# Performance work log

Measured on AMD Instinct MI355X. Metric: run time of the kernel, lower is better.

Reference implementation:

```python
import jax, jax.numpy as jnp
import numpy as np

BN_EPS = 1e-5


def setup_inputs() -> dict:
    key = jax.random.key(0)
    ks = jax.random.split(key, 8)
    N, E, D, G, L = 50000, 800000, 128, 64, 4
    x = jax.random.normal(ks[0], (N, D), dtype=jnp.float32)
    edge_index = jax.random.randint(ks[1], (2, E), 0, N, dtype=jnp.int64)
    batch = jnp.sort(jax.random.randint(ks[2], (N,), 0, G, dtype=jnp.int64))
    sc = 1.0 / np.sqrt(D)
    W1 = jax.random.normal(ks[3], (L, D, D), dtype=jnp.float32) * sc
    b1 = jnp.zeros((L, D), dtype=jnp.float32)
    gamma = jnp.ones((L, D), dtype=jnp.float32)
    beta = jnp.zeros((L, D), dtype=jnp.float32)
    W2 = jax.random.normal(ks[4], (L, D, D), dtype=jnp.float32) * sc
    b2 = jnp.zeros((L, D), dtype=jnp.float32)
    return {"x": x, "edge_index": edge_index, "batch": batch,
            "W1": W1, "b1": b1, "gamma": gamma, "beta": beta,
            "W2": W2, "b2": b2}


def _segment_mean(vals, ids, num_segments):
    s = jax.ops.segment_sum(vals, ids, num_segments=num_segments)
    cnt = jax.ops.segment_sum(jnp.ones((vals.shape[0],), vals.dtype), ids,
                              num_segments=num_segments)
    return s / jnp.clip(cnt, 1.0)[:, None]


def reference(x, edge_index, batch, W1, b1, gamma, beta, W2, b2):
    N = x.shape[0]
    L = W1.shape[0]
    G = 64  # number of graphs
    src, dst = edge_index[0], edge_index[1]  # source_to_target flow
    # in-degree counts for scatter-mean (fixed across layers)
    deg = jax.ops.segment_sum(jnp.ones((src.shape[0],), x.dtype), dst,
                              num_segments=N)
    deg = jnp.clip(deg, 1.0)[:, None]
    h = x
    node_pool = jnp.zeros((N, W1.shape[2]), x.dtype)
    g_pool = jnp.zeros((G, W1.shape[2]), x.dtype)
    for l in range(L):
        # scatter-mean neighbor aggregation, GIN update with eps=0
        agg = jax.ops.segment_sum(h[src], dst, num_segments=N) / deg
        z = h + agg
        # MLP: Linear -> BatchNorm1d (batch stats) -> ReLU -> Linear
        z = z @ W1[l] + b1[l]
        mu = jnp.mean(z, axis=0)
        var = jnp.mean(jnp.square(z - mu), axis=0)  # biased, as in torch BN
        z = gamma[l] * (z - mu) * jax.lax.rsqrt(var + BN_EPS) + beta[l]
        z = jax.nn.relu(z)
        h = z @ W2[l] + b2[l]
        node_pool = node_pool + h
        g_pool = g_pool + _segment_mean(h, batch, G)
    return node_pool, g_pool
```

## Files before the change

### kernel.cpp

```cpp
#include <hip/hip_runtime.h>

#define D 128
#define GNUM 64
#define LNUM 4
#define BN_EPS 1e-5f
#define EPB 16384
#define SH_MAX 12544

typedef short bf16x8 __attribute__((ext_vector_type(8)));
typedef float f32x4 __attribute__((ext_vector_type(4)));
typedef unsigned short u16x8 __attribute__((ext_vector_type(8)));
typedef unsigned short u16x4 __attribute__((ext_vector_type(4)));

__device__ __forceinline__ float bf2f(unsigned short u) {
  union { unsigned int i; float f; } v; v.i = ((unsigned int)u) << 16; return v.f;
}
__device__ __forceinline__ unsigned short f2bf(float f) {
  union { float f; unsigned int i; } v; v.f = f;
  unsigned int b = v.i;
  return (unsigned short)((b + 0x7FFFu + ((b >> 16) & 1u)) >> 16);
}


__global__ __launch_bounds__(256) void k_hist(const int* __restrict__ ei, int E,
                                              int B, int nbin, int* __restrict__ hist) {
  __shared__ int lh[256];
  int b = blockIdx.x, tx = threadIdx.x;
  lh[tx] = 0;
  __syncthreads();
  int s = b * EPB, e = min(s + EPB, E);
  for (int j = s + tx; j < e; j += 256) atomicAdd(&lh[ei[(size_t)E + j] >> 8], 1);
  __syncthreads();
  if (tx < nbin) hist[tx * B + b] = lh[tx];
}

__global__ __launch_bounds__(1024) void k_hscan(const int* __restrict__ hist, int M,
                                                int* __restrict__ off,
                                                int* __restrict__ rowptr, int N, int E) {
  __shared__ int sh[SH_MAX];
  __shared__ int sh2[1024];
  int tx = threadIdx.x;
  int chunk = (M + 1023) / 1024;
  for (int i = 0; i < chunk; ++i) {
    int idx = tx * chunk + i;
    sh[idx] = (idx < M) ? hist[idx] : 0;
  }
  __syncthreads();
  int s = 0;
  for (int i = 0; i < chunk; ++i) s += sh[tx * chunk + i];
  sh2[tx] = s;
  __syncthreads();
  for (int o = 1; o < 1024; o <<= 1) {
    int u = (tx >= o) ? sh2[tx - o] : 0;
    __syncthreads();
    sh2[tx] += u;
    __syncthreads();
  }
  int run = (tx == 0) ? 0 : sh2[tx - 1];
  for (int i = 0; i < chunk; ++i) {
    int idx = tx * chunk + i;
    if (idx < M) { int v = sh[idx]; off[idx] = run; run += v; }
  }
  if (tx == 0) rowptr[N] = E;
}

__global__ __launch_bounds__(256) void k_scatter(const int* __restrict__ ei, int E,
                                                 int B, int nbin,
                                                 const int* __restrict__ off,
                                                 int2* __restrict__ sorted) {
  __shared__ int cur[256];
  int b = blockIdx.x, tx = threadIdx.x;
  if (tx < nbin) cur[tx] = off[tx * B + b];
  __syncthreads();
  int s = b * EPB, e = min(s + EPB, E);
  for (int j = s + tx; j < e; j += 256) {
    int d = ei[(size_t)E + j];
    int sc = ei[j];
    int p = atomicAdd(&cur[d >> 8], 1);
    sorted[p] = make_int2(d, sc);
  }
}

__global__ __launch_bounds__(256) void k_build(const int2* __restrict__ sorted,
                                               const int* __restrict__ off,
                                               int B, int nbin, int E, int N,
                                               int* __restrict__ rowptr,
                                               int* __restrict__ col) {
  __shared__ int cnt[256], excl[256], cur[256];
  int beta = blockIdx.x, tx = threadIdx.x;
  int s = off[beta * B];
  int e = (beta + 1 < nbin) ? off[(beta + 1) * B] : E;
  cnt[tx] = 0;
  __syncthreads();
  for (int j = s + tx; j < e; j += 256) atomicAdd(&cnt[sorted[j].x & 255], 1);
  __syncthreads();
  int v = cnt[tx];
  excl[tx] = v;
  __syncthreads();
  for (int o = 1; o < 256; o <<= 1) {
    int u = (tx >= o) ? excl[tx - o] : 0;
    __syncthreads();
    excl[tx] += u;
    __syncthreads();
  }
  int ex = excl[tx] - v;
  int n = beta * 256 + tx;
  if (n < N) rowptr[n] = s + ex;
  cur[tx] = s + ex;
  __syncthreads();
  for (int j = s + tx; j < e; j += 256) {
    int2 p = sorted[j];
    int q = atomicAdd(&cur[p.x & 255], 1);
    col[q] = p.y;
  }
}

__global__ void k_bounds(const int* __restrict__ batch, int N, int* __restrict__ bound) {
  int g = threadIdx.x;
  if (g > GNUM) return;
  int lo = 0, hi = N;
  while (lo < hi) { int mid = (lo + hi) >> 1; if (batch[mid] < g) lo = mid + 1; else hi = mid; }
  bound[g] = lo;
}

__global__ void k_prep_x(const float* __restrict__ x, unsigned short* __restrict__ hx, int total4) {
  int i = blockIdx.x * 256 + threadIdx.x;
  if (i < total4) {
    f32x4 v = ((const f32x4*)x)[i];
    u16x4 o; o[0] = f2bf(v[0]); o[1] = f2bf(v[1]); o[2] = f2bf(v[2]); o[3] = f2bf(v[3]);
    ((u16x4*)hx)[i] = o;
  }
}

__global__ __launch_bounds__(256) void k_prep_w(const float* __restrict__ W1,
                                                const float* __restrict__ W2,
                                                unsigned short* __restrict__ wt) {
  int l = blockIdx.x;
  const float* W = (l < LNUM) ? (W1 + (size_t)l * D * D) : (W2 + (size_t)(l - LNUM) * D * D);
  unsigned short* o = wt + (size_t)l * D * D;
#pragma unroll
  for (int i = 0; i < 64; ++i) {
    int idx = threadIdx.x + 256 * i;
    int k = idx >> 7, n = idx & 127;
    o[n * D + k] = f2bf(W[idx]);
  }
}

__global__ __launch_bounds__(256) void k_aggz(const unsigned short* __restrict__ hin,
                                              const int* __restrict__ rowptr,
                                              const int* __restrict__ col,
                                              int N, unsigned short* __restrict__ z) {
  int tx = threadIdx.x;
  int w = tx >> 6, l = tx & 63;
  int g = l >> 4;
  int c = l & 15;
  int n = blockIdx.x * 4 + w;
  if (n >= N) return;
  int e0 = rowptr[n], e1 = rowptr[n + 1];
  const u16x8* h8 = (const u16x8*)hin;
  f32x4 a0 = {0.f, 0.f, 0.f, 0.f}, a1 = {0.f, 0.f, 0.f, 0.f};
  f32x4 b0 = {0.f, 0.f, 0.f, 0.f}, b1 = {0.f, 0.f, 0.f, 0.f};
  int j = e0 + g;
  for (; j + 4 < e1; j += 8) {
    int cj0 = col[j];
    int cj1 = col[j + 4];
    u16x8 v0 = h8[(size_t)cj0 * 16 + c];
    u16x8 v1 = h8[(size_t)cj1 * 16 + c];
    a0[0] += bf2f(v0[0]); a0[1] += bf2f(v0[1]); a0[2] += bf2f(v0[2]); a0[3] += bf2f(v0[3]);
    a1[0] += bf2f(v0[4]); a1[1] += bf2f(v0[5]); a1[2] += bf2f(v0[6]); a1[3] += bf2f(v0[7]);
    b0[0] += bf2f(v1[0]); b0[1] += bf2f(v1[1]); b0[2] += bf2f(v1[2]); b0[3] += bf2f(v1[3]);
    b1[0] += bf2f(v1[4]); b1[1] += bf2f(v1[5]); b1[2] += bf2f(v1[6]); b1[3] += bf2f(v1[7]);
  }
  if (j < e1) {
    int cj = col[j];
    u16x8 v = h8[(size_t)cj * 16 + c];
    a0[0] += bf2f(v[0]); a0[1] += bf2f(v[1]); a0[2] += bf2f(v[2]); a0[3] += bf2f(v[3]);
    a1[0] += bf2f(v[4]); a1[1] += bf2f(v[5]); a1[2] += bf2f(v[6]); a1[3] += bf2f(v[7]);
  }
  a0 += b0; a1 += b1;
#pragma unroll
  for (int m = 16; m <= 32; m <<= 1) {
#pragma unroll
    for (int i = 0; i < 4; ++i) {
      a0[i] += __shfl_xor(a0[i], m, 64);
      a1[i] += __shfl_xor(a1[i], m, 64);
    }
  }
  if (g == 0) {
    float inv = (e1 > e0) ? 1.f / (float)(e1 - e0) : 0.f;
    u16x8 hv = h8[(size_t)n * 16 + c];
    u16x8 o;
    o[0] = f2bf(bf2f(hv[0]) + a0[0] * inv);
    o[1] = f2bf(bf2f(hv[1]) + a0[1] * inv);
    o[2] = f2bf(bf2f(hv[2]) + a0[2] * inv);
    o[3] = f2bf(bf2f(hv[3]) + a0[3] * inv);
    o[4] = f2bf(bf2f(hv[4]) + a1[0] * inv);
    o[5] = f2bf(bf2f(hv[5]) + a1[1] * inv);
    o[6] = f2bf(bf2f(hv[6]) + a1[2] * inv);
    o[7] = f2bf(bf2f(hv[7]) + a1[3] * inv);
    ((u16x8*)z)[(size_t)n * 16 + c] = o;
  }
}

__global__ __launch_bounds__(256) void k_gemm1(const unsigned short* __restrict__ z,
                                               const unsigned short* __restrict__ wt,
                                               const float* __restrict__ bias,
                                               unsigned short* __restrict__ t,
                                               float* __restrict__ partials, int N) {
  __shared__ union { unsigned short zt[64 * D]; float red[2 * 8 * D]; } uA;
  __shared__ union { unsigned short wl[D * D]; float out[64 * D]; } uB;
  int tx = threadIdx.x;
  int r0 = blockIdx.x * 64;
  const u16x8* zg = (const u16x8*)(z + (size_t)r0 * D);
#pragma unroll
  for (int i = 0; i < 4; ++i) {
    int cid = tx + 256 * i;
    int row = cid >> 4, c16 = cid & 15;
    u16x8 v = zg[cid];
    *(u16x8*)((char*)uA.zt + row * 256 + ((c16 * 16) ^ ((row & 7) << 4))) = v;
  }
  const u16x8* wg = (const u16x8*)wt;
#pragma unroll
  for (int i = 0; i < 8; ++i) {
    int cid = tx + 256 * i;
    int row = cid >> 4, c16 = cid & 15;
    u16x8 v = wg[cid];
    *(u16x8*)((char*)uB.wl + row * 256 + ((c16 * 16) ^ ((row & 7) << 4))) = v;
  }
  __syncthreads();
  int l = tx & 63, w = tx >> 6;
  int lm = l & 15, lg = l >> 4;
  f32x4 acc[8];
#pragma unroll
  for (int c = 0; c < 8; ++c) { float bv = bias[c * 16 + lm]; acc[c] = (f32x4){bv, bv, bv, bv}; }
  int arow = 16 * w + lm;
  const char* zb = (const char*)uA.zt + arow * 256;
  int aswz = (arow & 7) << 4;
#pragma unroll
  for (int kt = 0; kt < 4; ++kt) {
    int koff = kt * 64 + lg * 16;
    bf16x8 af = *(const bf16x8*)(zb + (koff ^ aswz));
#pragma unroll
    for (int c = 0; c < 8; ++c) {
      int n = c * 16 + lm;
      bf16x8 bfr = *(const bf16x8*)((const char*)uB.wl + n * 256 + (koff ^ ((n & 7) << 4)));
      acc[c] = __builtin_amdgcn_mfma_f32_16x16x32_bf16(af, bfr, acc[c], 0, 0, 0);
    }
  }
  __syncthreads();
#pragma unroll
  for (int c = 0; c < 8; ++c)
#pragma unroll
    for (int r = 0; r < 4; ++r)
      uB.out[(16 * w + 4 * lg + r) * D + c * 16 + lm] = acc[c][r];
  __syncthreads();
  int tc = tx & 31, tr = tx >> 5;
  f32x4 s = {0.f, 0.f, 0.f, 0.f}, q = {0.f, 0.f, 0.f, 0.f};
#pragma unroll
  for (int i = 0; i < 8; ++i) {
    int row = i * 8 + tr;
    f32x4 v = *(f32x4*)&uB.out[row * D + tc * 4];
    u16x4 o; o[0] = f2bf(v[0]); o[1] = f2bf(v[1]); o[2] = f2bf(v[2]); o[3] = f2bf(v[3]);
    *(u16x4*)(t + (size_t)(r0 + row) * D + tc * 4) = o;
    if (r0 + row < N) { s += v; q += v * v; }
  }
  *(f32x4*)&uA.red[tr * D + tc * 4] = s;
  *(f32x4*)&uA.red[8 * D + tr * D + tc * 4] = q;
  __syncthreads();
  int colx = tx & 127, which = tx >> 7;
  float S = 0.f;
#pragma unroll
  for (int j = 0; j < 8; ++j) S += uA.red[which * 8 * D + j * D + colx];
  partials[(size_t)blockIdx.x * 256 + tx] = S;
}

__global__ __launch_bounds__(256) void k_red1(const float* __restrict__ partials, int NB,
                                              float* __restrict__ partial2) {
  int tx = threadIdx.x;
  float S = 0.f;
  for (int b = blockIdx.x; b < NB; b += 64) S += partials[(size_t)b * 256 + tx];
  partial2[(size_t)blockIdx.x * 256 + tx] = S;
}

__global__ __launch_bounds__(256) void k_finalize(const float* __restrict__ partial2,
                                                  const float* __restrict__ gamma,
                                                  const float* __restrict__ beta,
                                                  float* __restrict__ stats, int N) {
  __shared__ float sh[256];
  int tx = threadIdx.x;
  float S = 0.f;
#pragma unroll 8
  for (int b = 0; b < 64; ++b) S += partial2[(size_t)b * 256 + tx];
  sh[tx] = S;
  __syncthreads();
  if (tx < D) {
    float mu = sh[tx] / (float)N;
    float var = sh[D + tx] / (float)N - mu * mu;
    float rstd = rsqrtf(fmaxf(var, 0.f) + BN_EPS);
    float A = gamma[tx] * rstd;
    stats[tx] = A;
    stats[D + tx] = beta[tx] - mu * A;
  }
}

__global__ __launch_bounds__(256) void k_gemm2(const unsigned short* __restrict__ t,
                                               const unsigned short* __restrict__ wt,
                                               const float* __restrict__ bias,
                                               const float* __restrict__ stats,
                                               unsigned short* __restrict__ h,
                                               float* __restrict__ node_pool, int N) {
  __shared__ unsigned short at[64 * D];
  __shared__ union { unsigned short wl[D * D]; float out[64 * D]; } uB;
  int tx = threadIdx.x;
  int r0 = blockIdx.x * 64;
  const u16x8* tg = (const u16x8*)(t + (size_t)r0 * D);
#pragma unroll
  for (int i = 0; i < 4; ++i) {
    int cid = tx + 256 * i;
    int row = cid >> 4, c16 = cid & 15;
    u16x8 v = tg[cid];
    int c0 = c16 * 8;
    f32x4 a0 = *(const f32x4*)&stats[c0];
    f32x4 a1 = *(const f32x4*)&stats[c0 + 4];
    f32x4 b0 = *(const f32x4*)&stats[D + c0];
    f32x4 b1v = *(const f32x4*)&stats[D + c0 + 4];
    u16x8 o;
    o[0] = f2bf(fmaxf(bf2f(v[0]) * a0[0] + b0[0], 0.f));
    o[1] = f2bf(fmaxf(bf2f(v[1]) * a0[1] + b0[1], 0.f));
    o[2] = f2bf(fmaxf(bf2f(v[2]) * a0[2] + b0[2], 0.f));
    o[3] = f2bf(fmaxf(bf2f(v[3]) * a0[3] + b0[3], 0.f));
    o[4] = f2bf(fmaxf(bf2f(v[4]) * a1[0] + b1v[0], 0.f));
    o[5] = f2bf(fmaxf(bf2f(v[5]) * a1[1] + b1v[1], 0.f));
    o[6] = f2bf(fmaxf(bf2f(v[6]) * a1[2] + b1v[2], 0.f));
    o[7] = f2bf(fmaxf(bf2f(v[7]) * a1[3] + b1v[3], 0.f));
    *(u16x8*)((char*)at + row * 256 + ((c16 * 16) ^ ((row & 7) << 4))) = o;
  }
  const u16x8* wg = (const u16x8*)wt;
#pragma unroll
  for (int i = 0; i < 8; ++i) {
    int cid = tx + 256 * i;
    int row = cid >> 4, c16 = cid & 15;
    u16x8 v = wg[cid];
    *(u16x8*)((char*)uB.wl + row * 256 + ((c16 * 16) ^ ((row & 7) << 4))) = v;
  }
  __syncthreads();
  int l = tx & 63, w = tx >> 6;
  int lm = l & 15, lg = l >> 4;
  f32x4 acc[8];
#pragma unroll
  for (int c = 0; c < 8; ++c) { float bv = bias[c * 16 + lm]; acc[c] = (f32x4){bv, bv, bv, bv}; }
  int arow = 16 * w + lm;
  const char* ab = (const char*)at + arow * 256;
  int aswz = (arow & 7) << 4;
#pragma unroll
  for (int kt = 0; kt < 4; ++kt) {
    int koff = kt * 64 + lg * 16;
    bf16x8 af = *(const bf16x8*)(ab + (koff ^ aswz));
#pragma unroll
    for (int c = 0; c < 8; ++c) {
      int n = c * 16 + lm;
      bf16x8 bfr = *(const bf16x8*)((const char*)uB.wl + n * 256 + (koff ^ ((n & 7) << 4)));
      acc[c] = __builtin_amdgcn_mfma_f32_16x16x32_bf16(af, bfr, acc[c], 0, 0, 0);
    }
  }
  __syncthreads();
#pragma unroll
  for (int c = 0; c < 8; ++c)
#pragma unroll
    for (int r = 0; r < 4; ++r)
      uB.out[(16 * w + 4 * lg + r) * D + c * 16 + lm] = acc[c][r];
  __syncthreads();
  int tc = tx & 31, tr = tx >> 5;
#pragma unroll
  for (int i = 0; i < 8; ++i) {
    int row = i * 8 + tr;
    int gr = r0 + row;
    if (gr < N) {
      f32x4 v = *(f32x4*)&uB.out[row * D + tc * 4];
      f32x4* np = (f32x4*)(node_pool + (size_t)gr * D + tc * 4);
      f32x4 o = *np;
      o += v;
      *np = o;
      u16x4 hb; hb[0] = f2bf(v[0]); hb[1] = f2bf(v[1]); hb[2] = f2bf(v[2]); hb[3] = f2bf(v[3]);
      *(u16x4*)(h + (size_t)gr * D + tc * 4) = hb;
    }
  }
}

__global__ __launch_bounds__(256) void k_gpool(const float* __restrict__ np,
                                               const int* __restrict__ bound,
                                               float* __restrict__ gp) {
  __shared__ float red[8 * D];
  int g = blockIdx.x;
  int s = bound[g], e = bound[g + 1];
  int tc = threadIdx.x & 31, tr = threadIdx.x >> 5;
  f32x4 a = {0.f, 0.f, 0.f, 0.f};
  for (int r = s + tr; r < e; r += 8)
    a += *(const f32x4*)(np + (size_t)r * D + tc * 4);
  *(f32x4*)&red[tr * D + tc * 4] = a;
  __syncthreads();
  if (threadIdx.x < D) {
    float v = 0.f;
#pragma unroll
    for (int j = 0; j < 8; ++j) v += red[j * D + threadIdx.x];
    float c = (float)(e - s);
    gp[(size_t)g * D + threadIdx.x] = v / fmaxf(c, 1.f);
  }
}

extern "C" void kernel_launch(void* const* d_in, const int* in_sizes, int n_in,
                              void* d_out, int out_size, void* d_ws,
                              size_t ws_size, hipStream_t stream) {
  const float* x = (const float*)d_in[0];
  const int* ei = (const int*)d_in[1];
  const int* batch = (const int*)d_in[2];
  const float* W1 = (const float*)d_in[3];
  const float* b1 = (const float*)d_in[4];
  const float* gamma = (const float*)d_in[5];
  const float* beta = (const float*)d_in[6];
  const float* W2 = (const float*)d_in[7];
  const float* b2 = (const float*)d_in[8];
  int N = in_sizes[0] / D;
  int E = in_sizes[1] / 2;
  int Npad = (N + 63) & ~63;
  int gb = Npad / 64;
  int B = (E + EPB - 1) / EPB;
  int nbin = (N + 255) / 256;
  int M = nbin * B;

  float* out = (float*)d_out;
  float* node_pool = out;
  float* g_pool = out + (size_t)N * D;

  char* wp = (char*)d_ws;
  unsigned short* t_hx = (unsigned short*)wp; wp += (size_t)Npad * D * 2;
  unsigned short* h = (unsigned short*)wp;    wp += (size_t)Npad * D * 2;
  unsigned short* z = (unsigned short*)wp;    wp += (size_t)Npad * D * 2;
  unsigned short* wt = (unsigned short*)wp;   wp += (size_t)8 * D * D * 2;
  float* partials = (float*)wp;               wp += (size_t)gb * 256 * 4;
  float* partial2 = (float*)wp;               wp += (size_t)64 * 256 * 4;
  float* stats = (float*)wp;                  wp += (size_t)2 * D * 4;
  int* bound = (int*)wp;                      wp += (size_t)(GNUM + 4) * 4;
  int* rowptr = (int*)wp;                     wp += (size_t)(N + 1) * 4;
  int* hist = (int*)wp;                       wp += (size_t)SH_MAX * 4;
  int* off = (int*)wp;                        wp += (size_t)SH_MAX * 4;
  int* col = (int*)wp;                        wp += (size_t)E * 4;
  int2* sorted = (int2*)wp;                   wp += (size_t)E * 8;

  hipMemsetAsync(node_pool, 0, (size_t)N * D * 4, stream);
  if (Npad > N) {
    size_t padB = (size_t)(Npad - N) * D * 2;
    hipMemsetAsync(t_hx + (size_t)N * D, 0, padB, stream);
    hipMemsetAsync(h + (size_t)N * D, 0, padB, stream);
    hipMemsetAsync(z + (size_t)N * D, 0, padB, stream);
  }

  k_prep_w<<<8, 256, 0, stream>>>(W1, W2, wt);
  k_prep_x<<<(N * 32 + 255) / 256, 256, 0, stream>>>(x, t_hx, N * 32);
  k_hist<<<B, 256, 0, stream>>>(ei, E, B, nbin, hist);
  k_hscan<<<1, 1024, 0, stream>>>(hist, M, off, rowptr, N, E);
  k_scatter<<<B, 256, 0, stream>>>(ei, E, B, nbin, off, sorted);
  k_build<<<nbin, 256, 0, stream>>>(sorted, off, B, nbin, E, N, rowptr, col);
  k_bounds<<<1, 128, 0, stream>>>(batch, N, bound);

  int ab = (N + 3) / 4;
  for (int ll = 0; ll < LNUM; ++ll) {
    const unsigned short* hin = (ll == 0) ? t_hx : h;
    k_aggz<<<ab, 256, 0, stream>>>(hin, rowptr, col, N, z);
    k_gemm1<<<gb, 256, 0, stream>>>(z, wt + (size_t)ll * D * D, b1 + (size_t)ll * D,
                                    t_hx, partials, N);
    k_red1<<<64, 256, 0, stream>>>(partials, gb, partial2);
    k_finalize<<<1, 256, 0, stream>>>(partial2, gamma + (size_t)ll * D,
                                      beta + (size_t)ll * D, stats, N);
    k_gemm2<<<gb, 256, 0, stream>>>(t_hx, wt + (size_t)(LNUM + ll) * D * D,
                                    b2 + (size_t)ll * D, stats, h, node_pool, N);
  }
  k_gpool<<<GNUM, 256, 0, stream>>>(node_pool, bound, g_pool);
}
```

Before: 450.4 us.

## Defer node_pool accumulation to one final kernel and unroll neighbor gather

Each layer's bf16 output h now goes to its own buffer, and k_gemm2 no longer does a read-modify-write of the fp32 node_pool. A new k_npool kernel sums the four bf16 layer outputs once at the end and writes node_pool, which also removes the zeroing memset of node_pool. The aggregation loop in k_aggz is unrolled to four independent neighbor loads and accumulators per iteration, giving more loads in flight. The cost is more workspace, and node_pool is now summed from bf16-rounded h rather than fp32 values, which slightly lowers precision.

```diff
diff --git a/kernel.cpp b/kernel.cpp
--- a/kernel.cpp
+++ b/kernel.cpp
@@ -160,24 +160,35 @@
   const u16x8* h8 = (const u16x8*)hin;
   f32x4 a0 = {0.f, 0.f, 0.f, 0.f}, a1 = {0.f, 0.f, 0.f, 0.f};
   f32x4 b0 = {0.f, 0.f, 0.f, 0.f}, b1 = {0.f, 0.f, 0.f, 0.f};
+  f32x4 c0 = {0.f, 0.f, 0.f, 0.f}, c1 = {0.f, 0.f, 0.f, 0.f};
+  f32x4 d0 = {0.f, 0.f, 0.f, 0.f}, d1 = {0.f, 0.f, 0.f, 0.f};
   int j = e0 + g;
-  for (; j + 4 < e1; j += 8) {
+  for (; j + 12 < e1; j += 16) {
     int cj0 = col[j];
     int cj1 = col[j + 4];
+    int cj2 = col[j + 8];
+    int cj3 = col[j + 12];
     u16x8 v0 = h8[(size_t)cj0 * 16 + c];
     u16x8 v1 = h8[(size_t)cj1 * 16 + c];
+    u16x8 v2 = h8[(size_t)cj2 * 16 + c];
+    u16x8 v3 = h8[(size_t)cj3 * 16 + c];
     a0[0] += bf2f(v0[0]); a0[1] += bf2f(v0[1]); a0[2] += bf2f(v0[2]); a0[3] += bf2f(v0[3]);
     a1[0] += bf2f(v0[4]); a1[1] += bf2f(v0[5]); a1[2] += bf2f(v0[6]); a1[3] += bf2f(v0[7]);
     b0[0] += bf2f(v1[0]); b0[1] += bf2f(v1[1]); b0[2] += bf2f(v1[2]); b0[3] += bf2f(v1[3]);
     b1[0] += bf2f(v1[4]); b1[1] += bf2f(v1[5]); b1[2] += bf2f(v1[6]); b1[3] += bf2f(v1[7]);
-  }
-  if (j < e1) {
+    c0[0] += bf2f(v2[0]); c0[1] += bf2f(v2[1]); c0[2] += bf2f(v2[2]); c0[3] += bf2f(v2[3]);
+    c1[0] += bf2f(v2[4]); c1[1] += bf2f(v2[5]); c1[2] += bf2f(v2[6]); c1[3] += bf2f(v2[7]);
+    d0[0] += bf2f(v3[0]); d0[1] += bf2f(v3[1]); d0[2] += bf2f(v3[2]); d0[3] += bf2f(v3[3]);
+    d1[0] += bf2f(v3[4]); d1[1] += bf2f(v3[5]); d1[2] += bf2f(v3[6]); d1[3] += bf2f(v3[7]);
+  }
+  for (; j < e1; j += 4) {
     int cj = col[j];
     u16x8 v = h8[(size_t)cj * 16 + c];
     a0[0] += bf2f(v[0]); a0[1] += bf2f(v[1]); a0[2] += bf2f(v[2]); a0[3] += bf2f(v[3]);
     a1[0] += bf2f(v[4]); a1[1] += bf2f(v[5]); a1[2] += bf2f(v[6]); a1[3] += bf2f(v[7]);
   }
-  a0 += b0; a1 += b1;
+  a0 += b0; c0 += d0; a0 += c0;
+  a1 += b1; c1 += d1; a1 += c1;
 #pragma unroll
   for (int m = 16; m <= 32; m <<= 1) {
 #pragma unroll
@@ -307,8 +318,7 @@
                                                const unsigned short* __restrict__ wt,
                                                const float* __restrict__ bias,
                                                const float* __restrict__ stats,
-                                               unsigned short* __restrict__ h,
-                                               float* __restrict__ node_pool, int N) {
+                                               unsigned short* __restrict__ h, int N) {
   __shared__ unsigned short at[64 * D];
   __shared__ union { unsigned short wl[D * D]; float out[64 * D]; } uB;
   int tx = threadIdx.x;
@@ -377,14 +387,31 @@
     int gr = r0 + row;
     if (gr < N) {
       f32x4 v = *(f32x4*)&uB.out[row * D + tc * 4];
-      f32x4* np = (f32x4*)(node_pool + (size_t)gr * D + tc * 4);
-      f32x4 o = *np;
-      o += v;
-      *np = o;
       u16x4 hb; hb[0] = f2bf(v[0]); hb[1] = f2bf(v[1]); hb[2] = f2bf(v[2]); hb[3] = f2bf(v[3]);
       *(u16x4*)(h + (size_t)gr * D + tc * 4) = hb;
     }
   }
+}
+
+__global__ void k_npool(const unsigned short* __restrict__ h0,
+                        const unsigned short* __restrict__ h1,
+                        const unsigned short* __restrict__ h2,
+                        const unsigned short* __restrict__ h3,
+                        float* __restrict__ np, int total8) {
+  int i = blockIdx.x * 256 + threadIdx.x;
+  if (i >= total8) return;
+  u16x8 a = ((const u16x8*)h0)[i];
+  u16x8 b = ((const u16x8*)h1)[i];
+  u16x8 c = ((const u16x8*)h2)[i];
+  u16x8 d = ((const u16x8*)h3)[i];
+  f32x4 lo, hi;
+#pragma unroll
+  for (int j = 0; j < 4; ++j) {
+    lo[j] = (bf2f(a[j]) + bf2f(b[j])) + (bf2f(c[j]) + bf2f(d[j]));
+    hi[j] = (bf2f(a[4 + j]) + bf2f(b[4 + j])) + (bf2f(c[4 + j]) + bf2f(d[4 + j]));
+  }
+  ((f32x4*)np)[2 * i] = lo;
+  ((f32x4*)np)[2 * i + 1] = hi;
 }
 
 __global__ __launch_bounds__(256) void k_gpool(const float* __restrict__ np,
@@ -434,8 +461,9 @@
 
   char* wp = (char*)d_ws;
   unsigned short* t_hx = (unsigned short*)wp; wp += (size_t)Npad * D * 2;
-  unsigned short* h = (unsigned short*)wp;    wp += (size_t)Npad * D * 2;
   unsigned short* z = (unsigned short*)wp;    wp += (size_t)Npad * D * 2;
+  unsigned short* hbuf[LNUM];
+  for (int l = 0; l < LNUM; ++l) { hbuf[l] = (unsigned short*)wp; wp += (size_t)Npad * D * 2; }
   unsigned short* wt = (unsigned short*)wp;   wp += (size_t)8 * D * D * 2;
   float* partials = (float*)wp;               wp += (size_t)gb * 256 * 4;
   float* partial2 = (float*)wp;               wp += (size_t)64 * 256 * 4;
@@ -447,12 +475,8 @@
   int* col = (int*)wp;                        wp += (size_t)E * 4;
   int2* sorted = (int2*)wp;                   wp += (size_t)E * 8;
 
-  hipMemsetAsync(node_pool, 0, (size_t)N * D * 4, stream);
   if (Npad > N) {
-    size_t padB = (size_t)(Npad - N) * D * 2;
-    hipMemsetAsync(t_hx + (size_t)N * D, 0, padB, stream);
-    hipMemsetAsync(h + (size_t)N * D, 0, padB, stream);
-    hipMemsetAsync(z + (size_t)N * D, 0, padB, stream);
+    hipMemsetAsync(z + (size_t)N * D, 0, (size_t)(Npad - N) * D * 2, stream);
   }
 
   k_prep_w<<<8, 256, 0, stream>>>(W1, W2, wt);
@@ -465,7 +489,7 @@
 
   int ab = (N + 3) / 4;
   for (int ll = 0; ll < LNUM; ++ll) {
-    const unsigned short* hin = (ll == 0) ? t_hx : h;
+    const unsigned short* hin = (ll == 0) ? t_hx : hbuf[ll - 1];
     k_aggz<<<ab, 256, 0, stream>>>(hin, rowptr, col, N, z);
     k_gemm1<<<gb, 256, 0, stream>>>(z, wt + (size_t)ll * D * D, b1 + (size_t)ll * D,
                                     t_hx, partials, N);
@@ -473,7 +497,10 @@
     k_finalize<<<1, 256, 0, stream>>>(partial2, gamma + (size_t)ll * D,
                                       beta + (size_t)ll * D, stats, N);
     k_gemm2<<<gb, 256, 0, stream>>>(t_hx, wt + (size_t)(LNUM + ll) * D * D,
-                                    b2 + (size_t)ll * D, stats, h, node_pool, N);
-  }
+                                    b2 + (size_t)ll * D, stats, hbuf[ll], N);
+  }
+  int total8 = N * (D / 8);
+  k_npool<<<(total8 + 255) / 256, 256, 0, stream>>>(hbuf[0], hbuf[1], hbuf[2], hbuf[3],
+                                                    node_pool, total8);
   k_gpool<<<GNUM, 256, 0, stream>>>(node_pool, bound, g_pool);
 }
```

After: 458.7 us. Within noise of the previous version (+1.8%).

## Fuse neighbor aggregation into first GEMM and defer node_pool accumulation

Applied to the files above, without the earlier changes.

Aggregation of neighbor features is moved into the first GEMM kernel, so each block gathers its 64 rows directly into shared memory instead of going through a global z buffer. Per-layer fp32 node_pool read-modify-write is replaced by keeping each layer's bf16 output in its own buffer and summing all four in the final GEMM2 epilogue. This removes z round-trips, several memsets, and three full fp32 RMW passes. In exchange, gather parallelism per row drops and LDS-heavy blocks may limit latency hiding, and earlier-layer contributions to node_pool are bf16-rounded.

```diff
diff --git a/kernel.cpp b/kernel.cpp
--- a/kernel.cpp
+++ b/kernel.cpp
@@ -20,7 +20,6 @@
   unsigned int b = v.i;
   return (unsigned short)((b + 0x7FFFu + ((b >> 16) & 1u)) >> 16);
 }
-
 
 __global__ __launch_bounds__(256) void k_hist(const int* __restrict__ ei, int E,
                                               int B, int nbin, int* __restrict__ hist) {
@@ -146,79 +145,17 @@
   }
 }
 
-__global__ __launch_bounds__(256) void k_aggz(const unsigned short* __restrict__ hin,
-                                              const int* __restrict__ rowptr,
-                                              const int* __restrict__ col,
-                                              int N, unsigned short* __restrict__ z) {
-  int tx = threadIdx.x;
-  int w = tx >> 6, l = tx & 63;
-  int g = l >> 4;
-  int c = l & 15;
-  int n = blockIdx.x * 4 + w;
-  if (n >= N) return;
-  int e0 = rowptr[n], e1 = rowptr[n + 1];
-  const u16x8* h8 = (const u16x8*)hin;
-  f32x4 a0 = {0.f, 0.f, 0.f, 0.f}, a1 = {0.f, 0.f, 0.f, 0.f};
-  f32x4 b0 = {0.f, 0.f, 0.f, 0.f}, b1 = {0.f, 0.f, 0.f, 0.f};
-  int j = e0 + g;
-  for (; j + 4 < e1; j += 8) {
-    int cj0 = col[j];
-    int cj1 = col[j + 4];
-    u16x8 v0 = h8[(size_t)cj0 * 16 + c];
-    u16x8 v1 = h8[(size_t)cj1 * 16 + c];
-    a0[0] += bf2f(v0[0]); a0[1] += bf2f(v0[1]); a0[2] += bf2f(v0[2]); a0[3] += bf2f(v0[3]);
-    a1[0] += bf2f(v0[4]); a1[1] += bf2f(v0[5]); a1[2] += bf2f(v0[6]); a1[3] += bf2f(v0[7]);
-    b0[0] += bf2f(v1[0]); b0[1] += bf2f(v1[1]); b0[2] += bf2f(v1[2]); b0[3] += bf2f(v1[3]);
-    b1[0] += bf2f(v1[4]); b1[1] += bf2f(v1[5]); b1[2] += bf2f(v1[6]); b1[3] += bf2f(v1[7]);
-  }
-  if (j < e1) {
-    int cj = col[j];
-    u16x8 v = h8[(size_t)cj * 16 + c];
-    a0[0] += bf2f(v[0]); a0[1] += bf2f(v[1]); a0[2] += bf2f(v[2]); a0[3] += bf2f(v[3]);
-    a1[0] += bf2f(v[4]); a1[1] += bf2f(v[5]); a1[2] += bf2f(v[6]); a1[3] += bf2f(v[7]);
-  }
-  a0 += b0; a1 += b1;
-#pragma unroll
-  for (int m = 16; m <= 32; m <<= 1) {
-#pragma unroll
-    for (int i = 0; i < 4; ++i) {
-      a0[i] += __shfl_xor(a0[i], m, 64);
-      a1[i] += __shfl_xor(a1[i], m, 64);
-    }
-  }
-  if (g == 0) {
-    float inv = (e1 > e0) ? 1.f / (float)(e1 - e0) : 0.f;
-    u16x8 hv = h8[(size_t)n * 16 + c];
-    u16x8 o;
-    o[0] = f2bf(bf2f(hv[0]) + a0[0] * inv);
-    o[1] = f2bf(bf2f(hv[1]) + a0[1] * inv);
-    o[2] = f2bf(bf2f(hv[2]) + a0[2] * inv);
-    o[3] = f2bf(bf2f(hv[3]) + a0[3] * inv);
-    o[4] = f2bf(bf2f(hv[4]) + a1[0] * inv);
-    o[5] = f2bf(bf2f(hv[5]) + a1[1] * inv);
-    o[6] = f2bf(bf2f(hv[6]) + a1[2] * inv);
-    o[7] = f2bf(bf2f(hv[7]) + a1[3] * inv);
-    ((u16x8*)z)[(size_t)n * 16 + c] = o;
-  }
-}
-
-__global__ __launch_bounds__(256) void k_gemm1(const unsigned short* __restrict__ z,
-                                               const unsigned short* __restrict__ wt,
-                                               const float* __restrict__ bias,
-                                               unsigned short* __restrict__ t,
-                                               float* __restrict__ partials, int N) {
+__global__ __launch_bounds__(256) void k_layer1(const unsigned short* __restrict__ hin,
+                                                const int* __restrict__ rowptr,
+                                                const int* __restrict__ col,
+                                                const unsigned short* __restrict__ wt,
+                                                const float* __restrict__ bias,
+                                                unsigned short* __restrict__ t,
+                                                float* __restrict__ partials, int N) {
   __shared__ union { unsigned short zt[64 * D]; float red[2 * 8 * D]; } uA;
   __shared__ union { unsigned short wl[D * D]; float out[64 * D]; } uB;
   int tx = threadIdx.x;
   int r0 = blockIdx.x * 64;
-  const u16x8* zg = (const u16x8*)(z + (size_t)r0 * D);
-#pragma unroll
-  for (int i = 0; i < 4; ++i) {
-    int cid = tx + 256 * i;
-    int row = cid >> 4, c16 = cid & 15;
-    u16x8 v = zg[cid];
-    *(u16x8*)((char*)uA.zt + row * 256 + ((c16 * 16) ^ ((row & 7) << 4))) = v;
-  }
   const u16x8* wg = (const u16x8*)wt;
 #pragma unroll
   for (int i = 0; i < 8; ++i) {
@@ -227,12 +164,55 @@
     u16x8 v = wg[cid];
     *(u16x8*)((char*)uB.wl + row * 256 + ((c16 * 16) ^ ((row & 7) << 4))) = v;
   }
+  int grp = tx >> 4, c = tx & 15;
+  const u16x8* h8 = (const u16x8*)hin;
+#pragma unroll
+  for (int i = 0; i < 4; ++i) {
+    int row = grp * 4 + i;
+    int n = r0 + row;
+    u16x8 o;
+    if (n < N) {
+      int e0 = rowptr[n], e1 = rowptr[n + 1];
+      f32x4 s0 = {0.f,0.f,0.f,0.f}, s1 = {0.f,0.f,0.f,0.f};
+      f32x4 t0 = {0.f,0.f,0.f,0.f}, t1 = {0.f,0.f,0.f,0.f};
+      int j = e0;
+      for (; j + 3 < e1; j += 4) {
+        u16x8 v0 = h8[(size_t)col[j] * 16 + c];
+        u16x8 v1 = h8[(size_t)col[j + 1] * 16 + c];
+        u16x8 v2 = h8[(size_t)col[j + 2] * 16 + c];
+        u16x8 v3 = h8[(size_t)col[j + 3] * 16 + c];
+#pragma unroll
+        for (int k = 0; k < 4; ++k) {
+          s0[k] += bf2f(v0[k]) + bf2f(v1[k]);
+          s1[k] += bf2f(v0[4 + k]) + bf2f(v1[4 + k]);
+          t0[k] += bf2f(v2[k]) + bf2f(v3[k]);
+          t1[k] += bf2f(v2[4 + k]) + bf2f(v3[4 + k]);
+        }
+      }
+      for (; j < e1; ++j) {
+        u16x8 v0 = h8[(size_t)col[j] * 16 + c];
+#pragma unroll
+        for (int k = 0; k < 4; ++k) { s0[k] += bf2f(v0[k]); s1[k] += bf2f(v0[4 + k]); }
+      }
+      s0 += t0; s1 += t1;
+      float inv = (e1 > e0) ? 1.f / (float)(e1 - e0) : 0.f;
+      u16x8 hv = h8[(size_t)n * 16 + c];
+#pragma unroll
+      for (int k = 0; k < 4; ++k) {
+        o[k] = f2bf(bf2f(hv[k]) + s0[k] * inv);
+        o[4 + k] = f2bf(bf2f(hv[4 + k]) + s1[k] * inv);
+      }
+    } else {
+      o = (u16x8){0, 0, 0, 0, 0, 0, 0, 0};
+    }
+    *(u16x8*)((char*)uA.zt + row * 256 + ((c * 16) ^ ((row & 7) << 4))) = o;
+  }
   __syncthreads();
   int l = tx & 63, w = tx >> 6;
   int lm = l & 15, lg = l >> 4;
   f32x4 acc[8];
 #pragma unroll
-  for (int c = 0; c < 8; ++c) { float bv = bias[c * 16 + lm]; acc[c] = (f32x4){bv, bv, bv, bv}; }
+  for (int cc = 0; cc < 8; ++cc) { float bv = bias[cc * 16 + lm]; acc[cc] = (f32x4){bv, bv, bv, bv}; }
   int arow = 16 * w + lm;
   const char* zb = (const char*)uA.zt + arow * 256;
   int aswz = (arow & 7) << 4;
@@ -241,18 +221,18 @@
     int koff = kt * 64 + lg * 16;
     bf16x8 af = *(const bf16x8*)(zb + (koff ^ aswz));
 #pragma unroll
-    for (int c = 0; c < 8; ++c) {
-      int n = c * 16 + lm;
+    for (int cc = 0; cc < 8; ++cc) {
+      int n = cc * 16 + lm;
       bf16x8 bfr = *(const bf16x8*)((const char*)uB.wl + n * 256 + (koff ^ ((n & 7) << 4)));
-      acc[c] = __builtin_amdgcn_mfma_f32_16x16x32_bf16(af, bfr, acc[c], 0, 0, 0);
-    }
-  }
-  __syncthreads();
-#pragma unroll
-  for (int c = 0; c < 8; ++c)
+      acc[cc] = __builtin_amdgcn_mfma_f32_16x16x32_bf16(af, bfr, acc[cc], 0, 0, 0);
+    }
+  }
+  __syncthreads();
+#pragma unroll
+  for (int cc = 0; cc < 8; ++cc)
 #pragma unroll
     for (int r = 0; r < 4; ++r)
-      uB.out[(16 * w + 4 * lg + r) * D + c * 16 + lm] = acc[c][r];
+      uB.out[(16 * w + 4 * lg + r) * D + cc * 16 + lm] = acc[cc][r];
   __syncthreads();
   int tc = tx & 31, tr = tx >> 5;
   f32x4 s = {0.f, 0.f, 0.f, 0.f}, q = {0.f, 0.f, 0.f, 0.f};
@@ -303,16 +283,12 @@
   }
 }
 
-__global__ __launch_bounds__(256) void k_gemm2(const unsigned short* __restrict__ t,
-                                               const unsigned short* __restrict__ wt,
-                                               const float* __restrict__ bias,
-                                               const float* __restrict__ stats,
-                                               unsigned short* __restrict__ h,
-                                               float* __restrict__ node_pool, int N) {
-  __shared__ unsigned short at[64 * D];
-  __shared__ union { unsigned short wl[D * D]; float out[64 * D]; } uB;
-  int tx = threadIdx.x;
-  int r0 = blockIdx.x * 64;
+__device__ __forceinline__ void gemm2_core(const unsigned short* t,
+                                           const unsigned short* wt,
+                                           const float* bias, const float* stats,
+                                           unsigned short* at, unsigned short* wl,
+                                           float* outbuf, int r0) {
+  int tx = threadIdx.x;
   const u16x8* tg = (const u16x8*)(t + (size_t)r0 * D);
 #pragma unroll
   for (int i = 0; i < 4; ++i) {
@@ -341,7 +317,7 @@
     int cid = tx + 256 * i;
     int row = cid >> 4, c16 = cid & 15;
     u16x8 v = wg[cid];
-    *(u16x8*)((char*)uB.wl + row * 256 + ((c16 * 16) ^ ((row & 7) << 4))) = v;
+    *(u16x8*)((char*)wl + row * 256 + ((c16 * 16) ^ ((row & 7) << 4))) = v;
   }
   __syncthreads();
   int l = tx & 63, w = tx >> 6;
@@ -359,7 +335,7 @@
 #pragma unroll
     for (int c = 0; c < 8; ++c) {
       int n = c * 16 + lm;
-      bf16x8 bfr = *(const bf16x8*)((const char*)uB.wl + n * 256 + (koff ^ ((n & 7) << 4)));
+      bf16x8 bfr = *(const bf16x8*)((const char*)wl + n * 256 + (koff ^ ((n & 7) << 4)));
       acc[c] = __builtin_amdgcn_mfma_f32_16x16x32_bf16(af, bfr, acc[c], 0, 0, 0);
     }
   }
@@ -368,8 +344,20 @@
   for (int c = 0; c < 8; ++c)
 #pragma unroll
     for (int r = 0; r < 4; ++r)
-      uB.out[(16 * w + 4 * lg + r) * D + c * 16 + lm] = acc[c][r];
-  __syncthreads();
+      outbuf[(16 * w + 4 * lg + r) * D + c * 16 + lm] = acc[c][r];
+  __syncthreads();
+}
+
+__global__ __launch_bounds__(256) void k_gemm2(const unsigned short* __restrict__ t,
+                                               const unsigned short* __restrict__ wt,
+                                               const float* __restrict__ bias,
+                                               const float* __restrict__ stats,
+                                               unsigned short* __restrict__ h, int N) {
+  __shared__ unsigned short at[64 * D];
+  __shared__ union { unsigned short wl[D * D]; float out[64 * D]; } uB;
+  int tx = threadIdx.x;
+  int r0 = blockIdx.x * 64;
+  gemm2_core(t, wt, bias, stats, at, uB.wl, uB.out, r0);
   int tc = tx & 31, tr = tx >> 5;
 #pragma unroll
   for (int i = 0; i < 8; ++i) {
@@ -377,12 +365,41 @@
     int gr = r0 + row;
     if (gr < N) {
       f32x4 v = *(f32x4*)&uB.out[row * D + tc * 4];
-      f32x4* np = (f32x4*)(node_pool + (size_t)gr * D + tc * 4);
-      f32x4 o = *np;
-      o += v;
-      *np = o;
       u16x4 hb; hb[0] = f2bf(v[0]); hb[1] = f2bf(v[1]); hb[2] = f2bf(v[2]); hb[3] = f2bf(v[3]);
       *(u16x4*)(h + (size_t)gr * D + tc * 4) = hb;
+    }
+  }
+}
+
+__global__ __launch_bounds__(256) void k_gemm2_last(const unsigned short* __restrict__ t,
+                                                    const unsigned short* __restrict__ wt,
+                                                    const float* __restrict__ bias,
+                                                    const float* __restrict__ stats,
+                                                    const unsigned short* __restrict__ h0,
+                                                    const unsigned short* __restrict__ h1,
+                                                    const unsigned short* __restrict__ h2,
+                                                    float* __restrict__ np, int N) {
+  __shared__ unsigned short at[64 * D];
+  __shared__ union { unsigned short wl[D * D]; float out[64 * D]; } uB;
+  int tx = threadIdx.x;
+  int r0 = blockIdx.x * 64;
+  gemm2_core(t, wt, bias, stats, at, uB.wl, uB.out, r0);
+  int tc = tx & 31, tr = tx >> 5;
+#pragma unroll
+  for (int i = 0; i < 8; ++i) {
+    int row = i * 8 + tr;
+    int gr = r0 + row;
+    if (gr < N) {
+      f32x4 v = *(f32x4*)&uB.out[row * D + tc * 4];
+      size_t o4 = (size_t)gr * D + tc * 4;
+      u16x4 a = *(const u16x4*)(h0 + o4);
+      u16x4 b = *(const u16x4*)(h1 + o4);
+      u16x4 cc = *(const u16x4*)(h2 + o4);
+      f32x4 o;
+#pragma unroll
+      for (int k = 0; k < 4; ++k)
+        o[k] = v[k] + (bf2f(a[k]) + bf2f(b[k])) + bf2f(cc[k]);
+      *(f32x4*)(np + o4) = o;
     }
   }
 }
@@ -433,9 +450,10 @@
   float* g_pool = out + (size_t)N * D;
 
   char* wp = (char*)d_ws;
-  unsigned short* t_hx = (unsigned short*)wp; wp += (size_t)Npad * D * 2;
-  unsigned short* h = (unsigned short*)wp;    wp += (size_t)Npad * D * 2;
-  unsigned short* z = (unsigned short*)wp;    wp += (size_t)Npad * D * 2;
+  unsigned short* hx = (unsigned short*)wp;   wp += (size_t)Npad * D * 2;
+  unsigned short* t = (unsigned short*)wp;    wp += (size_t)Npad * D * 2;
+  unsigned short* hbuf[3];
+  for (int l = 0; l < 3; ++l) { hbuf[l] = (unsigned short*)wp; wp += (size_t)Npad * D * 2; }
   unsigned short* wt = (unsigned short*)wp;   wp += (size_t)8 * D * D * 2;
   float* partials = (float*)wp;               wp += (size_t)gb * 256 * 4;
   float* partial2 = (float*)wp;               wp += (size_t)64 * 256 * 4;
@@ -447,33 +465,29 @@
   int* col = (int*)wp;                        wp += (size_t)E * 4;
   int2* sorted = (int2*)wp;                   wp += (size_t)E * 8;
 
-  hipMemsetAsync(node_pool, 0, (size_t)N * D * 4, stream);
-  if (Npad > N) {
-    size_t padB = (size_t)(Npad - N) * D * 2;
-    hipMemsetAsync(t_hx + (size_t)N * D, 0, padB, stream);
-    hipMemsetAsync(h + (size_t)N * D, 0, padB, stream);
-    hipMemsetAsync(z + (size_t)N * D, 0, padB, stream);
-  }
-
   k_prep_w<<<8, 256, 0, stream>>>(W1, W2, wt);
-  k_prep_x<<<(N * 32 + 255) / 256, 256, 0, stream>>>(x, t_hx, N * 32);
+  k_prep_x<<<(N * 32 + 255) / 256, 256, 0, stream>>>(x, hx, N * 32);
   k_hist<<<B, 256, 0, stream>>>(ei, E, B, nbin, hist);
   k_hscan<<<1, 1024, 0, stream>>>(hist, M, off, rowptr, N, E);
   k_scatter<<<B, 256, 0, stream>>>(ei, E, B, nbin, off, sorted);
   k_build<<<nbin, 256, 0, stream>>>(sorted, off, B, nbin, E, N, rowptr, col);
   k_bounds<<<1, 128, 0, stream>>>(batch, N, bound);
 
-  int ab = (N + 3) / 4;
   for (int ll = 0; ll < LNUM; ++ll) {
-    const unsigned short* hin = (ll == 0) ? t_hx : h;
-    k_aggz<<<ab, 256, 0, stream>>>(hin, rowptr, col, N, z);
-    k_gemm1<<<gb, 256, 0, stream>>>(z, wt + (size_t)ll * D * D, b1 + (size_t)ll * D,
-                                    t_hx, partials, N);
+    const unsigned short* hin = (ll == 0) ? hx : hbuf[ll - 1];
+    k_layer1<<<gb, 256, 0, stream>>>(hin, rowptr, col, wt + (size_t)ll * D * D,
+                                     b1 + (size_t)ll * D, t, partials, N);
     k_red1<<<64, 256, 0, stream>>>(partials, gb, partial2);
     k_finalize<<<1, 256, 0, stream>>>(partial2, gamma + (size_t)ll * D,
                                       beta + (size_t)ll * D, stats, N);
-    k_gemm2<<<gb, 256, 0, stream>>>(t_hx, wt + (size_t)(LNUM + ll) * D * D,
-                                    b2 + (size_t)ll * D, stats, h, node_pool, N);
+    if (ll < LNUM - 1) {
+      k_gemm2<<<gb, 256, 0, stream>>>(t, wt + (size_t)(LNUM + ll) * D * D,
+                                      b2 + (size_t)ll * D, stats, hbuf[ll], N);
+    } else {
+      k_gemm2_last<<<gb, 256, 0, stream>>>(t, wt + (size_t)(LNUM + ll) * D * D,
+                                           b2 + (size_t)ll * D, stats,
+                                           hbuf[0], hbuf[1], hbuf[2], node_pool, N);
+    }
   }
   k_gpool<<<GNUM, 256, 0, stream>>>(node_pool, bound, g_pool);
 }
```

New measurement: 458.7 us. No clear change (+1.8%).
